# Kernel optimization log

Measured on AMD Instinct MI355X. Metric: run time of the kernel, lower is better.

## Reference

```python
import jax, jax.numpy as jnp
import numpy as np


def setup_inputs() -> dict:
    key = jax.random.key(0)
    ks = jax.random.split(key, 10)
    B, T, D = 256, 256, 256
    CH, L, K = 128, 3, 10          # chunk_size, levels, conv_size
    H = CH * L                     # hidden_dim = 384
    G = 4 * H + 2 * L              # gate projection width = 1542
    HS = H // 6

    def xavier(k, shape):
        fan_in, fan_out = shape[0], shape[-1]
        lim = np.sqrt(6.0 / (fan_in + fan_out)).astype(np.float32)
        return jax.random.uniform(k, shape, jnp.float32, -lim, lim)

    x = jax.random.normal(ks[0], (B, T, D), jnp.float32)
    lengths = jax.random.randint(ks[1], (B,), 1, T + 1).astype(jnp.int64)
    Wk = xavier(ks[2], (D + 1, G)); bk = jnp.zeros((G,), jnp.float32)
    Wr = xavier(ks[3], (H + 1, G)); br = jnp.zeros((G,), jnp.float32)
    Ws = xavier(ks[4], (H, HS));    bs = jnp.zeros((HS,), jnp.float32)
    Wrs = xavier(ks[5], (HS, H));   brs = jnp.zeros((H,), jnp.float32)
    Wc = xavier(ks[6], (H, H, K)) / np.sqrt(K)  # Conv1d weight (out, in, k)
    bc = jnp.zeros((H,), jnp.float32)
    return {"x": x, "lengths": lengths, "Wk": Wk, "bk": bk, "Wr": Wr,
            "br": br, "Ws": Ws, "bs": bs, "Wrs": Wrs, "brs": brs,
            "Wc": Wc, "bc": bc}


def _cumax_l2r(z):
    return jnp.cumsum(jax.nn.softmax(z, axis=-1), axis=-1)


def _cumax_r2l(z):
    zf = jnp.flip(z, -1)
    return jnp.flip(jnp.cumsum(jax.nn.softmax(zf, axis=-1), axis=-1), -1)


def reference(x, lengths, Wk, bk, Wr, br, Ws, bs, Wrs, brs, Wc, bc):
    B, T, D = x.shape
    H = Wr.shape[0] - 1
    G = Wk.shape[1]
    L = (G - 4 * H) // 2
    CH = H // L
    K = Wc.shape[2]
    ones = jnp.ones((B, 1), x.dtype)

    def step(carry, xt):
        c, h, tmp_h, tmp_dis = carry
        # two linear projections (interval == 1 always)
        xo = (jnp.concatenate([xt, ones], -1) @ Wk + bk
              + jnp.concatenate([h, ones], -1) @ Wr + br)
        fm = _cumax_l2r(xo[:, :L])[:, :, None]          # (B,L,1)
        im = _cumax_r2l(xo[:, L:2 * L])[:, :, None]     # (B,L,1)
        rest = xo[:, 2 * L:].reshape(B, 4 * L, CH)
        f = jax.nn.sigmoid(rest[:, :L])
        i = jax.nn.sigmoid(rest[:, L:2 * L])
        o = jax.nn.sigmoid(rest[:, 2 * L:3 * L])
        c_in = jnp.tanh(rest[:, 3 * L:])
        c_last = c.reshape(B, L, CH)
        ov = fm * im
        c_new = (ov * (f * c_last + i * c_in)
                 + (fm - ov) * c_last + (im - ov) * c_in)
        h_new = (o * jnp.tanh(c_new)).reshape(B, H)
        c_new = c_new.reshape(B, H)
        cur_dis = 1.0 - jnp.mean(fm[..., 0], axis=-1)   # (B,)
        # sliding buffers (K, B, H) and (K, B)
        tmp_h = jnp.concatenate([tmp_h[1:], h_new[None]], 0)
        tmp_dis = jnp.concatenate([tmp_dis[1:], cur_dis[None]], 0)
        # local window attention weights
        ld = jax.nn.softmax(jnp.cumsum(tmp_dis.T, axis=1), axis=1)  # (B,K)
        local_h = tmp_h.transpose(1, 2, 0) * ld[:, None, :]         # (B,H,K)
        theme = jax.nn.sigmoid(
            jax.nn.relu(jnp.mean(local_h, -1) @ Ws + bs) @ Wrs + brs)
        conv = jnp.einsum('bhk,ohk->bo', local_h, Wc) + bc          # valid conv -> len 1
        local_out = theme * conv
        return (c_new, h_new, tmp_h, tmp_dis), (h_new, local_out)

    c0 = jnp.zeros((B, H), x.dtype)
    h0 = jnp.zeros((B, H), x.dtype)
    th0 = jnp.zeros((K, B, H), x.dtype)
    td0 = jnp.zeros((K, B), x.dtype)
    _, (origin_h, loc_h) = jax.lax.scan(step, (c0, h0, th0, td0),
                                        x.transpose(1, 0, 2))
    output = (loc_h + origin_h).transpose(1, 0, 2)   # (B,T,H)
    idx = jnp.clip(lengths, 1, T).astype(jnp.int32) - 1
    last_output = output[jnp.arange(B), idx]
    return (last_output, output)
```

## Files before the change

kernel.cpp:

```cpp
#include <hip/hip_runtime.h>
#include <hip/hip_bf16.h>
#include <cstddef>

#define B_  256
#define T_  256
#define D_  256
#define H_  384
#define G_  1542
#define L_  3
#define CH_ 128
#define K_  10
#define HS_ 64

#define NGRP 16
#define NMEM 16
#define GW   16
#define CPM  24
#define NFR  7
#define PCOLS 112
#define XOLP 114
#define NKC  20
#define STG_BYTES 12288
#define XOL_OFF   STG_BYTES
#define LDS_BYTES (STG_BYTES + XOLP * GW * 4)

#define POST_LDS 107520

#define SENT 0xFFFFFFFFFFFFFFFFull

using bf16x8 = __attribute__((ext_vector_type(8))) short;
using f32x4  = __attribute__((ext_vector_type(4))) float;
typedef unsigned long long ull_t;

__device__ __forceinline__ float bf2f(unsigned short s) {
    return __uint_as_float(((unsigned)s) << 16);
}
__device__ __forceinline__ unsigned short f2bf(float f) {
    unsigned u = __float_as_uint(f);
    return (unsigned short)((u + 0x7fffu + ((u >> 16) & 1u)) >> 16);
}
__device__ __forceinline__ float sig_fast(float x) { return 1.f / (1.f + __expf(-x)); }
__device__ __forceinline__ float tanh_fast(float x) {
    float ax = fabsf(x);
    float t = __expf(-2.f * ax);
    float r = (1.f - t) / (1.f + t);
    return copysignf(r, x);
}
__device__ __forceinline__ ull_t ldA(const ull_t* p) {
    return __hip_atomic_load(p, __ATOMIC_RELAXED, __HIP_MEMORY_SCOPE_AGENT);
}
__device__ __forceinline__ bool rdy(ull_t v) {
    ull_t x = ~v;
    return (((x - 0x0001000100010001ull) & ~x & 0x8000800080008000ull) == 0ull);
}

__device__ __forceinline__ int gcol_of(int member, int p) {
    if (p < 6) return p;
    if (p < 102) { int q = p - 6; return 6 + (q / CPM) * H_ + member * CPM + (q % CPM); }
    return -1;
}

__global__ __launch_bounds__(256)
void k_xa(const float* __restrict__ x, unsigned short* __restrict__ xA) {
    __shared__ float xl[64][261];
    const int t = blockIdx.x, bq = blockIdx.y;
    const int b0 = bq * 64, tid = threadIdx.x;
    for (int idx = tid; idx < 4096; idx += 256) {
        int row = idx >> 6, c4 = idx & 63;
        float4 v = *(const float4*)(x + ((size_t)(b0 + row) * T_ + t) * D_ + c4 * 4);
        xl[row][c4 * 4 + 0] = v.x; xl[row][c4 * 4 + 1] = v.y;
        xl[row][c4 * 4 + 2] = v.z; xl[row][c4 * 4 + 3] = v.w;
    }
    __syncthreads();
    for (int idx = tid; idx < 2048; idx += 256) {
        int lane = idx & 63, gl = (idx >> 6) & 3, kc = idx >> 8;
        int brow = gl * 16 + (lane & 15);
        int d = kc * 32 + (lane >> 4) * 8;
        unsigned o[4];
        #pragma unroll
        for (int q = 0; q < 4; ++q)
            o[q] = (unsigned)f2bf(xl[brow][d + 2 * q])
                 | ((unsigned)f2bf(xl[brow][d + 2 * q + 1]) << 16);
        int4 pk = make_int4((int)o[0], (int)o[1], (int)o[2], (int)o[3]);
        ((int4*)xA)[(((size_t)t * 8 + kc) * 16 + (bq * 4 + gl)) * 64 + lane] = pk;
    }
}

__global__ __launch_bounds__(256)
void k_prep(const float* __restrict__ Wk, const float* __restrict__ bk,
            const float* __restrict__ Wr, const float* __restrict__ br,
            const float* __restrict__ Ws, const float* __restrict__ Wrs,
            const float* __restrict__ Wc,
            unsigned short* __restrict__ hbf, unsigned short* __restrict__ Wf,
            unsigned short* __restrict__ Wg, unsigned short* __restrict__ WsT,
            unsigned short* __restrict__ WrsT, float* __restrict__ biasP)
{
    const int bid = blockIdx.x, tid = threadIdx.x;
    if (bid < 2048) {
        ull_t* hb = (ull_t*)hbf;
        int base = bid * 256 + tid;
        #pragma unroll
        for (int j = 0; j < 12; ++j)
            __hip_atomic_store(hb + base + j * 524288, SENT,
                               __ATOMIC_RELAXED, __HIP_MEMORY_SCOPE_AGENT);
    } else if (bid < 2608) {
        int idx = (bid - 2048) * 256 + tid;
        int lane = idx & 63;
        int ni   = (idx >> 6) % NFR;
        int kc   = (idx / (64 * NFR)) % NKC;
        int member = idx / (64 * NFR * NKC);
        int p = ni * 16 + (lane & 15);
        int g = gcol_of(member, p);
        unsigned short out[8];
        #pragma unroll
        for (int j = 0; j < 8; ++j) {
            int k = kc * 32 + (lane >> 4) * 8 + j;
            float v = 0.f;
            if (g >= 0) v = (k < 256) ? Wk[(size_t)k * G_ + g] : Wr[(size_t)(k - 256) * G_ + g];
            out[j] = f2bf(v);
        }
        int4 pk;
        pk.x = (unsigned)out[0] | ((unsigned)out[1] << 16);
        pk.y = (unsigned)out[2] | ((unsigned)out[3] << 16);
        pk.z = (unsigned)out[4] | ((unsigned)out[5] << 16);
        pk.w = (unsigned)out[6] | ((unsigned)out[7] << 16);
        ((int4*)Wf)[idx] = pk;
    } else if (bid < 8368) {
        int idx = (bid - 2608) * 256 + tid;
        int o = idx / (K_ * H_);
        int rem = idx % (K_ * H_);
        int k = rem / H_, h = rem % H_;
        Wg[idx] = f2bf(Wc[((size_t)o * H_ + h) * K_ + k]);
    } else if (bid < 8464) {
        int idx = (bid - 8368) * 256 + tid;
        int jj = idx / H_, k = idx % H_;
        WsT[idx] = f2bf(Ws[(size_t)k * HS_ + jj]);
    } else if (bid < 8560) {
        int idx = (bid - 8464) * 256 + tid;
        int o = idx / HS_, jj = idx % HS_;
        WrsT[idx] = f2bf(Wrs[(size_t)jj * H_ + o]);
    } else {
        int idx = (bid - 8560) * 256 + tid;
        if (idx < NMEM * PCOLS) {
            int member = idx / PCOLS, p = idx % PCOLS;
            int g = gcol_of(member, p);
            biasP[idx] = (g >= 0)
                ? bk[g] + br[g] + Wk[(size_t)256 * G_ + g] + Wr[(size_t)384 * G_ + g] : 0.f;
        }
    }
}

__global__ __launch_bounds__(512, 1)
void k_serial(const unsigned short* __restrict__ xA, const unsigned short* __restrict__ Wf,
              const float* __restrict__ biasP,
              unsigned short* __restrict__ hbf, float* __restrict__ dis)
{
    extern __shared__ char lds_raw[];
    int4* stage4 = (int4*)lds_raw;
    const bf16x8* stage = (const bf16x8*)lds_raw;
    float* xol = (float*)(lds_raw + XOL_OFF);

    const int tid = threadIdx.x;
    const int lane = tid & 63, wave = tid >> 6;
    const int group = blockIdx.x & 15, member = blockIdx.x >> 4;
    const int b0 = group * GW;
    const int ni = wave;
    const bool domm = (wave < NFR);

    bf16x8 wreg[NKC];
    if (domm) {
        const bf16x8* wsrc = (const bf16x8*)(Wf + (size_t)member * (NKC * NFR * 64 * 8));
        #pragma unroll
        for (int kc = 0; kc < NKC; ++kc)
            wreg[kc] = wsrc[(kc * NFR + ni) * 64 + lane];
    }
    const float bias_a = domm ? biasP[member * PCOLS + ni * 16 + (lane & 15)] : 0.f;

    const bool hasS = (tid < 384);
    const int skcl = tid >> 6, sln = tid & 63;
    const int stA = skcl * 64 + sln;
    const int stB = (skcl + 6) * 64 + sln;
    const unsigned short* src0 =
        hbf + (size_t)(b0 + (sln & 15)) * H_ + skcl * 32 + (sln >> 4) * 8;

    float c_r0 = 0.f;

    for (int t = 0; t < T_; ++t) {
        bf16x8 xf[8];
        if (domm) {
            #pragma unroll
            for (int kc = 0; kc < 8; ++kc)
                xf[kc] = *((const bf16x8*)(xA
                    + (((size_t)t * 8 + kc) * 16 + group) * 512 + lane * 8));
        }

        f32x4 accA = f32x4{bias_a, bias_a, bias_a, bias_a};
        f32x4 accB = f32x4{0.f, 0.f, 0.f, 0.f};

        if (t > 0) {
            const size_t toff = (size_t)(t - 1) * B_ * H_;
            const ull_t* pA = (const ull_t*)(src0 + toff);
            const ull_t* pB = (const ull_t*)(src0 + toff + 192);
            ull_t v0 = SENT, v1 = SENT, v2 = SENT, v3 = SENT;
            if (hasS) { v0 = ldA(pA); v1 = ldA(pA + 1); v2 = ldA(pB); v3 = ldA(pB + 1); }

            if (domm) {
                #pragma unroll
                for (int kc = 0; kc < 8; ++kc) {
                    if (kc & 1)
                        accB = __builtin_amdgcn_mfma_f32_16x16x32_bf16(xf[kc], wreg[kc], accB, 0, 0, 0);
                    else
                        accA = __builtin_amdgcn_mfma_f32_16x16x32_bf16(xf[kc], wreg[kc], accA, 0, 0, 0);
                }
            }

            if (hasS) {
                while (!(rdy(v0) && rdy(v1) && rdy(v2) && rdy(v3))) {
                    v0 = ldA(pA); v1 = ldA(pA + 1); v2 = ldA(pB); v3 = ldA(pB + 1);
                }
                stage4[stA] = make_int4((int)(v0 & 0xffffffffu), (int)(v0 >> 32),
                                        (int)(v1 & 0xffffffffu), (int)(v1 >> 32));
                stage4[stB] = make_int4((int)(v2 & 0xffffffffu), (int)(v2 >> 32),
                                        (int)(v3 & 0xffffffffu), (int)(v3 >> 32));
            }
            __syncthreads();
            if (domm) {
                #pragma unroll
                for (int kcl = 0; kcl < 12; ++kcl) {
                    bf16x8 a0 = stage[kcl * 64 + lane];
                    if (kcl & 1)
                        accB = __builtin_amdgcn_mfma_f32_16x16x32_bf16(a0, wreg[8 + kcl], accB, 0, 0, 0);
                    else
                        accA = __builtin_amdgcn_mfma_f32_16x16x32_bf16(a0, wreg[8 + kcl], accA, 0, 0, 0);
                }
            }
        } else {
            if (domm) {
                #pragma unroll
                for (int kc = 0; kc < 8; ++kc) {
                    if (kc & 1)
                        accB = __builtin_amdgcn_mfma_f32_16x16x32_bf16(xf[kc], wreg[kc], accB, 0, 0, 0);
                    else
                        accA = __builtin_amdgcn_mfma_f32_16x16x32_bf16(xf[kc], wreg[kc], accA, 0, 0, 0);
                }
            }
        }

        if (domm) {
            #pragma unroll
            for (int r = 0; r < 4; ++r)
                xol[((lane >> 4) * 4 + r) * XOLP + ni * 16 + (lane & 15)] = accA[r] + accB[r];
        }
        __syncthreads();

        if (tid < 384) {
            int b = tid & 15, ch = tid >> 4;
            const float* row = xol + b * XOLP;
            float z0 = row[0], z1 = row[1], z2 = row[2];
            float z3 = row[3], z4 = row[4], z5 = row[5];
            float m1 = fmaxf(fmaxf(z0, z1), z2);
            float e0 = __expf(z0 - m1), e1 = __expf(z1 - m1), e2 = __expf(z2 - m1);
            float inv1 = 1.f / (e0 + e1 + e2);
            float fm0 = e0 * inv1, fm1 = (e0 + e1) * inv1;
            float m2 = fmaxf(fmaxf(z3, z4), z5);
            float f3 = __expf(z3 - m2), f4 = __expf(z4 - m2), f5 = __expf(z5 - m2);
            float inv2 = 1.f / (f3 + f4 + f5);
            float im1 = (f4 + f5) * inv2, im2 = f5 * inv2;

            int hh = member * CPM + ch;
            int l = hh >> 7;
            float fm = (l == 0) ? fm0 : (l == 1) ? fm1 : 1.f;
            float im = (l == 0) ? 1.f : (l == 1) ? im1 : im2;

            float fg = sig_fast(row[6 + ch]);
            float ig = sig_fast(row[6 + CPM + ch]);
            float og = sig_fast(row[6 + 2 * CPM + ch]);
            float ci = tanh_fast(row[6 + 3 * CPM + ch]);

            float ov = fm * im;
            float cn = ov * (fg * c_r0 + ig * ci) + (fm - ov) * c_r0 + (im - ov) * ci;
            float hn = og * tanh_fast(cn);
            c_r0 = cn;

            unsigned hpk = (unsigned)f2bf(hn);
            unsigned partner = (unsigned)__shfl((int)hpk, (lane + 16) & 63);
            if (!(ch & 1)) {
                unsigned word = hpk | (partner << 16);
                __hip_atomic_store(
                    (unsigned*)(hbf + ((size_t)t * B_ + b0 + b) * H_ + hh),
                    word, __ATOMIC_RELAXED, __HIP_MEMORY_SCOPE_AGENT);
            }
            if (member == 0 && ch == 0)
                dis[t * B_ + b0 + b] = 1.f - (fm0 + fm1 + 1.f) * (1.f / 3.f);
        }
    }
}

__global__ __launch_bounds__(512, 1)
void k_post(const unsigned short* __restrict__ hbf, const float* __restrict__ dis,
            const unsigned short* __restrict__ Wg,
            const unsigned short* __restrict__ WsT, const unsigned short* __restrict__ WrsT,
            const float* __restrict__ bs, const float* __restrict__ brs,
            const float* __restrict__ bc, float* __restrict__ out_part)
{
    extern __shared__ char plds[];
    float* ldl = (float*)plds;
    unsigned short* AlB = (unsigned short*)(plds + 5120);
    unsigned short* BlB = (unsigned short*)(plds + 46080);
    unsigned short* hbarL = (unsigned short*)(plds + 5120);
    unsigned short* uL = (unsigned short*)(plds + 56320);

    const int bid = blockIdx.x + 4 * blockIdx.y;
    const int xcd = bid & 7, slot = bid >> 3;
    const int tpair = xcd * 16 + (slot >> 2);
    const int btile = slot & 3;
    const int b0 = btile * 64;
    const int t0 = tpair * 2;
    const int tid = threadIdx.x;
    const int wave = tid >> 6, lane = tid & 63;
    const int mh = wave >> 2, nq = wave & 3;

    if (tid < 128) {
        int ti = tid >> 6, bi = tid & 63;
        int t = t0 + ti, b = b0 + bi;
        float s = 0.f, sk[K_];
        #pragma unroll
        for (int k = 0; k < K_; ++k) {
            int tau = t - (K_ - 1) + k;
            float d = (tau >= 0) ? dis[tau * B_ + b] : 0.f;
            s += d; sk[k] = s;
        }
        float m = sk[0];
        #pragma unroll
        for (int k = 1; k < K_; ++k) m = fmaxf(m, sk[k]);
        float sum = 0.f;
        #pragma unroll
        for (int k = 0; k < K_; ++k) { sk[k] = __expf(sk[k] - m); sum += sk[k]; }
        float inv = 1.f / sum;
        #pragma unroll
        for (int k = 0; k < K_; ++k) ldl[ti * 640 + bi * 10 + k] = sk[k] * inv;
    }

    const int a_ti = tid >> 8, a_rem = tid & 255;
    const int a_bb = a_rem >> 2, a_half = a_rem & 3;

    auto loadA = [&](int ch, int4& av, bool& valid) {
        int k = ch / 12, hb = (ch % 12) * 32;
        int tau = t0 + a_ti - (K_ - 1) + k;
        valid = (tau >= 0);
        if (valid)
            av = *(const int4*)(hbf + ((size_t)tau * B_ + b0 + a_bb) * H_ + hb + a_half * 8);
    };
    auto loadB = [&](int ch, int4 bv[3]) {
        #pragma unroll
        for (int q = 0; q < 3; ++q) {
            int idx = q * 512 + tid;
            int row = idx >> 2, half = idx & 3;
            bv[q] = *(const int4*)(Wg + (size_t)row * 3840 + ch * 32 + half * 8);
        }
    };
    auto writeA = [&](int buf, int ch, int4 av, bool valid) {
        int k = ch / 12;
        int4 pk = make_int4(0, 0, 0, 0);
        if (valid) {
            float l = ldl[a_ti * 640 + a_bb * 10 + k];
            unsigned vv[4] = {(unsigned)av.x, (unsigned)av.y, (unsigned)av.z, (unsigned)av.w};
            unsigned o[4];
            #pragma unroll
            for (int q = 0; q < 4; ++q) {
                float flo = __uint_as_float(vv[q] << 16) * l;
                float fhi = __uint_as_float(vv[q] & 0xffff0000u) * l;
                o[q] = (unsigned)f2bf(flo) | ((unsigned)f2bf(fhi) << 16);
            }
            pk = make_int4((int)o[0], (int)o[1], (int)o[2], (int)o[3]);
        }
        *(int4*)&AlB[buf * 5120 + a_ti * 2560 + a_bb * 40 + a_half * 8] = pk;
    };
    auto writeB = [&](int buf, const int4 bv[3]) {
        #pragma unroll
        for (int q = 0; q < 3; ++q) {
            int idx = q * 512 + tid;
            int row = idx >> 2, half = idx & 3;
            *(int4*)&BlB[buf * 15360 + row * 40 + half * 8] = bv[q];
        }
    };

    int4 av; bool avalid; int4 bv[3];
    loadA(0, av, avalid); loadB(0, bv);
    __syncthreads();
    writeA(0, 0, av, avalid); writeB(0, bv);

    f32x4 acc[2][2][6] = {};
    for (int ch = 0; ch < 120; ++ch) {
        int cur = ch & 1;
        bool more = (ch + 1 < 120);
        if (more) { loadA(ch + 1, av, avalid); loadB(ch + 1, bv); }
        __syncthreads();
        if (more) { writeA(cur ^ 1, ch + 1, av, avalid); writeB(cur ^ 1, bv); }

        bf16x8 af[2][2];
        #pragma unroll
        for (int ti = 0; ti < 2; ++ti)
            #pragma unroll
            for (int mi = 0; mi < 2; ++mi)
                af[ti][mi] = *(const bf16x8*)&AlB[cur * 5120 + ti * 2560
                    + (mh * 32 + mi * 16 + (lane & 15)) * 40 + (lane >> 4) * 8];
        #pragma unroll
        for (int ni = 0; ni < 6; ++ni) {
            bf16x8 bfv = *(const bf16x8*)&BlB[cur * 15360
                + (nq * 96 + ni * 16 + (lane & 15)) * 40 + (lane >> 4) * 8];
            #pragma unroll
            for (int ti = 0; ti < 2; ++ti)
                #pragma unroll
                for (int mi = 0; mi < 2; ++mi)
                    acc[ti][mi][ni] = __builtin_amdgcn_mfma_f32_16x16x32_bf16(
                        af[ti][mi], bfv, acc[ti][mi][ni], 0, 0, 0);
        }
    }
    __syncthreads();

    #pragma unroll
    for (int ti = 0; ti < 2; ++ti) {
        const int t = t0 + ti;
        for (int idx = tid; idx < 3072; idx += 512) {
            int bb = idx / 48, h8 = idx % 48;
            float s[8] = {};
            #pragma unroll
            for (int k = 0; k < K_; ++k) {
                int tau = t - (K_ - 1) + k;
                if (tau >= 0) {
                    int4 v = *(const int4*)(hbf + ((size_t)tau * B_ + b0 + bb) * H_ + h8 * 8);
                    float l = ldl[ti * 640 + bb * 10 + k];
                    unsigned vv[4] = {(unsigned)v.x, (unsigned)v.y, (unsigned)v.z, (unsigned)v.w};
                    #pragma unroll
                    for (int q = 0; q < 4; ++q) {
                        s[2 * q]     = fmaf(__uint_as_float(vv[q] << 16), l, s[2 * q]);
                        s[2 * q + 1] = fmaf(__uint_as_float(vv[q] & 0xffff0000u), l, s[2 * q + 1]);
                    }
                }
            }
            unsigned o[4];
            #pragma unroll
            for (int q = 0; q < 4; ++q)
                o[q] = (unsigned)f2bf(s[2 * q] * 0.1f) | ((unsigned)f2bf(s[2 * q + 1] * 0.1f) << 16);
            *(int4*)&hbarL[bb * 400 + h8 * 8] = make_int4((int)o[0], (int)o[1], (int)o[2], (int)o[3]);
        }
        __syncthreads();

        if (wave < 4) {
            f32x4 uacc[4] = {};
            for (int kc = 0; kc < 12; ++kc) {
                bf16x8 a = *(const bf16x8*)&hbarL[(wave * 16 + (lane & 15)) * 400
                                                  + kc * 32 + (lane >> 4) * 8];
                #pragma unroll
                for (int ni = 0; ni < 4; ++ni) {
                    bf16x8 wb = *(const bf16x8*)(WsT + (size_t)(ni * 16 + (lane & 15)) * H_
                                                 + kc * 32 + (lane >> 4) * 8);
                    uacc[ni] = __builtin_amdgcn_mfma_f32_16x16x32_bf16(a, wb, uacc[ni], 0, 0, 0);
                }
            }
            #pragma unroll
            for (int ni = 0; ni < 4; ++ni) {
                float bsv = bs[ni * 16 + (lane & 15)];
                #pragma unroll
                for (int r = 0; r < 4; ++r)
                    uL[(wave * 16 + (lane >> 4) * 4 + r) * 72 + ni * 16 + (lane & 15)] =
                        f2bf(fmaxf(uacc[ni][r] + bsv, 0.f));
            }
        }
        __syncthreads();

        #pragma unroll
        for (int half = 0; half < 2; ++half) {
            f32x4 tacc[2][3] = {};
            #pragma unroll
            for (int kc = 0; kc < 2; ++kc) {
                bf16x8 ua[2];
                #pragma unroll
                for (int mi = 0; mi < 2; ++mi)
                    ua[mi] = *(const bf16x8*)&uL[(mh * 32 + mi * 16 + (lane & 15)) * 72
                                                 + kc * 32 + (lane >> 4) * 8];
                #pragma unroll
                for (int n3 = 0; n3 < 3; ++n3) {
                    int ni = half * 3 + n3;
                    bf16x8 wb = *(const bf16x8*)(WrsT
                        + (size_t)(nq * 96 + ni * 16 + (lane & 15)) * HS_
                        + kc * 32 + (lane >> 4) * 8);
                    #pragma unroll
                    for (int mi = 0; mi < 2; ++mi)
                        tacc[mi][n3] = __builtin_amdgcn_mfma_f32_16x16x32_bf16(
                            ua[mi], wb, tacc[mi][n3], 0, 0, 0);
                }
            }
            #pragma unroll
            for (int mi = 0; mi < 2; ++mi) {
                #pragma unroll
                for (int n3 = 0; n3 < 3; ++n3) {
                    int ni = half * 3 + n3;
                    int o = nq * 96 + ni * 16 + (lane & 15);
                    float brsv = brs[o], bcv = bc[o];
                    int brow0 = b0 + mh * 32 + mi * 16 + ((lane >> 4) << 2);
                    #pragma unroll
                    for (int r = 0; r < 4; ++r) {
                        float th = sig_fast(tacc[mi][n3][r] + brsv);
                        float cv = acc[ti][mi][ni][r] + bcv;
                        float hv = bf2f(hbf[((size_t)t * B_ + brow0 + r) * H_ + o]);
                        __builtin_nontemporal_store(hv + th * cv,
                            out_part + ((size_t)(brow0 + r) * T_ + t) * H_ + o);
                    }
                }
            }
        }
        __syncthreads();
    }
}

__global__ void k_last(const int* __restrict__ len_i, const float* __restrict__ out_part,
                       float* __restrict__ last)
{
    int b = blockIdx.x, tid = threadIdx.x;
    bool is64 = (len_i[1] == 0);
    long long v = is64 ? ((const long long*)len_i)[b] : (long long)len_i[b];
    int idx = (int)v;
    idx = max(1, min(T_, idx)) - 1;
    last[(size_t)b * H_ + tid] = out_part[((size_t)b * T_ + idx) * H_ + tid];
}

extern "C" void kernel_launch(void* const* d_in, const int* in_sizes, int n_in,
                              void* d_out, int out_size, void* d_ws, size_t ws_size,
                              hipStream_t stream) {
    const float* x   = (const float*)d_in[0];
    const int*   len = (const int*)d_in[1];
    const float* Wk  = (const float*)d_in[2];
    const float* bk  = (const float*)d_in[3];
    const float* Wr  = (const float*)d_in[4];
    const float* br  = (const float*)d_in[5];
    const float* Ws  = (const float*)d_in[6];
    const float* bs  = (const float*)d_in[7];
    const float* Wrs = (const float*)d_in[8];
    const float* brs = (const float*)d_in[9];
    const float* Wc  = (const float*)d_in[10];
    const float* bc  = (const float*)d_in[11];

    float* out      = (float*)d_out;
    float* last     = out;
    float* out_part = out + (size_t)B_ * H_;

    char* p = (char*)d_ws;
    float*          dis    = (float*)p;          p += (size_t)T_ * B_ * 4;
    unsigned short* xA     = (unsigned short*)p; p += (size_t)T_ * B_ * D_ * 2;
    unsigned short* WfragG = (unsigned short*)p; p += (size_t)NMEM * NKC * NFR * 64 * 8 * 2;
    float*          biasP  = (float*)p;          p += (size_t)NMEM * PCOLS * 4;
    unsigned short* hbf    = (unsigned short*)p; p += (size_t)T_ * B_ * H_ * 2;
    unsigned short* Wg     = (unsigned short*)p; p += (size_t)H_ * K_ * H_ * 2;
    unsigned short* WsT    = (unsigned short*)p; p += (size_t)HS_ * H_ * 2;
    unsigned short* WrsT   = (unsigned short*)p; p += (size_t)H_ * HS_ * 2;

    k_xa  <<<dim3(T_, 4), 256, 0, stream>>>(x, xA);
    k_prep<<<8567, 256, 0, stream>>>(Wk, bk, Wr, br, Ws, Wrs, Wc,
                                     hbf, WfragG, Wg, WsT, WrsT, biasP);

    hipFuncSetAttribute((const void*)k_serial,
                        hipFuncAttributeMaxDynamicSharedMemorySize, LDS_BYTES);
    hipFuncSetAttribute((const void*)k_post,
                        hipFuncAttributeMaxDynamicSharedMemorySize, POST_LDS);

    k_serial<<<NGRP * NMEM, 512, LDS_BYTES, stream>>>(xA, WfragG, biasP, hbf, dis);
    k_post <<<dim3(4, 128), 512, POST_LDS, stream>>>(hbf, dis, Wg, WsT, WrsT, bs, brs, bc, out_part);
    k_last <<<B_, H_, 0, stream>>>(len, out_part, last);
}
```

Before: 1.245 ms.

## Fuse serial recurrence and post-processing into one kernel with progress flags

Merges the serial recurrence kernel and the local-window post kernel into a single 512-block launch. The first 256 blocks run the recurrence and publish a per-group progress counter after each timestep. The remaining blocks wait on those counters and run the conv/theme post-processing for finished timesteps, so that work overlaps with the serial chain instead of running after it. The post stage's LDS budget is shrunk to fit (smaller B staging buffer) so both roles fit in one launch. This risks spin-wait contention and relies on all blocks being co-resident.

```diff
diff --git a/kernel.cpp b/kernel.cpp
--- a/kernel.cpp
+++ b/kernel.cpp
@@ -22,9 +22,7 @@
 #define NKC  20
 #define STG_BYTES 12288
 #define XOL_OFF   STG_BYTES
-#define LDS_BYTES (STG_BYTES + XOLP * GW * 4)
-
-#define POST_LDS 107520
+#define MAIN_LDS 65536
 
 #define SENT 0xFFFFFFFFFFFFFFFFull
 
@@ -93,7 +91,8 @@
             const float* __restrict__ Wc,
             unsigned short* __restrict__ hbf, unsigned short* __restrict__ Wf,
             unsigned short* __restrict__ Wg, unsigned short* __restrict__ WsT,
-            unsigned short* __restrict__ WrsT, float* __restrict__ biasP)
+            unsigned short* __restrict__ WrsT, float* __restrict__ biasP,
+            unsigned* __restrict__ progress)
 {
     const int bid = blockIdx.x, tid = threadIdx.x;
     if (bid < 2048) {
@@ -139,7 +138,7 @@
         int idx = (bid - 8464) * 256 + tid;
         int o = idx / HS_, jj = idx % HS_;
         WrsT[idx] = f2bf(Wrs[(size_t)jj * H_ + o]);
-    } else {
+    } else if (bid < 8567) {
         int idx = (bid - 8560) * 256 + tid;
         if (idx < NMEM * PCOLS) {
             int member = idx / PCOLS, p = idx % PCOLS;
@@ -147,371 +146,388 @@
             biasP[idx] = (g >= 0)
                 ? bk[g] + br[g] + Wk[(size_t)256 * G_ + g] + Wr[(size_t)384 * G_ + g] : 0.f;
         }
+    } else {
+        if (tid < NGRP * NMEM)
+            __hip_atomic_store(progress + tid, 0u,
+                               __ATOMIC_RELAXED, __HIP_MEMORY_SCOPE_AGENT);
     }
 }
 
 __global__ __launch_bounds__(512, 1)
-void k_serial(const unsigned short* __restrict__ xA, const unsigned short* __restrict__ Wf,
-              const float* __restrict__ biasP,
-              unsigned short* __restrict__ hbf, float* __restrict__ dis)
-{
-    extern __shared__ char lds_raw[];
-    int4* stage4 = (int4*)lds_raw;
-    const bf16x8* stage = (const bf16x8*)lds_raw;
-    float* xol = (float*)(lds_raw + XOL_OFF);
-
-    const int tid = threadIdx.x;
-    const int lane = tid & 63, wave = tid >> 6;
-    const int group = blockIdx.x & 15, member = blockIdx.x >> 4;
-    const int b0 = group * GW;
-    const int ni = wave;
-    const bool domm = (wave < NFR);
-
-    bf16x8 wreg[NKC];
-    if (domm) {
-        const bf16x8* wsrc = (const bf16x8*)(Wf + (size_t)member * (NKC * NFR * 64 * 8));
-        #pragma unroll
-        for (int kc = 0; kc < NKC; ++kc)
-            wreg[kc] = wsrc[(kc * NFR + ni) * 64 + lane];
-    }
-    const float bias_a = domm ? biasP[member * PCOLS + ni * 16 + (lane & 15)] : 0.f;
-
-    const bool hasS = (tid < 384);
-    const int skcl = tid >> 6, sln = tid & 63;
-    const int stA = skcl * 64 + sln;
-    const int stB = (skcl + 6) * 64 + sln;
-    const unsigned short* src0 =
-        hbf + (size_t)(b0 + (sln & 15)) * H_ + skcl * 32 + (sln >> 4) * 8;
-
-    float c_r0 = 0.f;
-
-    for (int t = 0; t < T_; ++t) {
-        bf16x8 xf[8];
-        if (domm) {
-            #pragma unroll
-            for (int kc = 0; kc < 8; ++kc)
-                xf[kc] = *((const bf16x8*)(xA
-                    + (((size_t)t * 8 + kc) * 16 + group) * 512 + lane * 8));
-        }
-
-        f32x4 accA = f32x4{bias_a, bias_a, bias_a, bias_a};
-        f32x4 accB = f32x4{0.f, 0.f, 0.f, 0.f};
-
-        if (t > 0) {
-            const size_t toff = (size_t)(t - 1) * B_ * H_;
-            const ull_t* pA = (const ull_t*)(src0 + toff);
-            const ull_t* pB = (const ull_t*)(src0 + toff + 192);
-            ull_t v0 = SENT, v1 = SENT, v2 = SENT, v3 = SENT;
-            if (hasS) { v0 = ldA(pA); v1 = ldA(pA + 1); v2 = ldA(pB); v3 = ldA(pB + 1); }
-
-            if (domm) {
-                #pragma unroll
-                for (int kc = 0; kc < 8; ++kc) {
-                    if (kc & 1)
-                        accB = __builtin_amdgcn_mfma_f32_16x16x32_bf16(xf[kc], wreg[kc], accB, 0, 0, 0);
-                    else
-                        accA = __builtin_amdgcn_mfma_f32_16x16x32_bf16(xf[kc], wreg[kc], accA, 0, 0, 0);
-                }
-            }
-
-            if (hasS) {
-                while (!(rdy(v0) && rdy(v1) && rdy(v2) && rdy(v3))) {
-                    v0 = ldA(pA); v1 = ldA(pA + 1); v2 = ldA(pB); v3 = ldA(pB + 1);
-                }
-                stage4[stA] = make_int4((int)(v0 & 0xffffffffu), (int)(v0 >> 32),
-                                        (int)(v1 & 0xffffffffu), (int)(v1 >> 32));
-                stage4[stB] = make_int4((int)(v2 & 0xffffffffu), (int)(v2 >> 32),
-                                        (int)(v3 & 0xffffffffu), (int)(v3 >> 32));
-            }
-            __syncthreads();
-            if (domm) {
-                #pragma unroll
-                for (int kcl = 0; kcl < 12; ++kcl) {
-                    bf16x8 a0 = stage[kcl * 64 + lane];
-                    if (kcl & 1)
-                        accB = __builtin_amdgcn_mfma_f32_16x16x32_bf16(a0, wreg[8 + kcl], accB, 0, 0, 0);
-                    else
-                        accA = __builtin_amdgcn_mfma_f32_16x16x32_bf16(a0, wreg[8 + kcl], accA, 0, 0, 0);
-                }
-            }
-        } else {
-            if (domm) {
-                #pragma unroll
-                for (int kc = 0; kc < 8; ++kc) {
-                    if (kc & 1)
-                        accB = __builtin_amdgcn_mfma_f32_16x16x32_bf16(xf[kc], wreg[kc], accB, 0, 0, 0);
-                    else
-                        accA = __builtin_amdgcn_mfma_f32_16x16x32_bf16(xf[kc], wreg[kc], accA, 0, 0, 0);
-                }
-            }
-        }
-
-        if (domm) {
-            #pragma unroll
-            for (int r = 0; r < 4; ++r)
-                xol[((lane >> 4) * 4 + r) * XOLP + ni * 16 + (lane & 15)] = accA[r] + accB[r];
-        }
-        __syncthreads();
-
-        if (tid < 384) {
-            int b = tid & 15, ch = tid >> 4;
-            const float* row = xol + b * XOLP;
-            float z0 = row[0], z1 = row[1], z2 = row[2];
-            float z3 = row[3], z4 = row[4], z5 = row[5];
-            float m1 = fmaxf(fmaxf(z0, z1), z2);
-            float e0 = __expf(z0 - m1), e1 = __expf(z1 - m1), e2 = __expf(z2 - m1);
-            float inv1 = 1.f / (e0 + e1 + e2);
-            float fm0 = e0 * inv1, fm1 = (e0 + e1) * inv1;
-            float m2 = fmaxf(fmaxf(z3, z4), z5);
-            float f3 = __expf(z3 - m2), f4 = __expf(z4 - m2), f5 = __expf(z5 - m2);
-            float inv2 = 1.f / (f3 + f4 + f5);
-            float im1 = (f4 + f5) * inv2, im2 = f5 * inv2;
-
-            int hh = member * CPM + ch;
-            int l = hh >> 7;
-            float fm = (l == 0) ? fm0 : (l == 1) ? fm1 : 1.f;
-            float im = (l == 0) ? 1.f : (l == 1) ? im1 : im2;
-
-            float fg = sig_fast(row[6 + ch]);
-            float ig = sig_fast(row[6 + CPM + ch]);
-            float og = sig_fast(row[6 + 2 * CPM + ch]);
-            float ci = tanh_fast(row[6 + 3 * CPM + ch]);
-
-            float ov = fm * im;
-            float cn = ov * (fg * c_r0 + ig * ci) + (fm - ov) * c_r0 + (im - ov) * ci;
-            float hn = og * tanh_fast(cn);
-            c_r0 = cn;
-
-            unsigned hpk = (unsigned)f2bf(hn);
-            unsigned partner = (unsigned)__shfl((int)hpk, (lane + 16) & 63);
-            if (!(ch & 1)) {
-                unsigned word = hpk | (partner << 16);
-                __hip_atomic_store(
-                    (unsigned*)(hbf + ((size_t)t * B_ + b0 + b) * H_ + hh),
-                    word, __ATOMIC_RELAXED, __HIP_MEMORY_SCOPE_AGENT);
-            }
-            if (member == 0 && ch == 0)
-                dis[t * B_ + b0 + b] = 1.f - (fm0 + fm1 + 1.f) * (1.f / 3.f);
-        }
-    }
-}
-
-__global__ __launch_bounds__(512, 1)
-void k_post(const unsigned short* __restrict__ hbf, const float* __restrict__ dis,
+void k_main(const unsigned short* __restrict__ xA, const unsigned short* __restrict__ Wf,
+            const float* __restrict__ biasP, unsigned short* __restrict__ hbf,
+            float* __restrict__ dis, unsigned* __restrict__ progress,
             const unsigned short* __restrict__ Wg,
             const unsigned short* __restrict__ WsT, const unsigned short* __restrict__ WrsT,
             const float* __restrict__ bs, const float* __restrict__ brs,
             const float* __restrict__ bc, float* __restrict__ out_part)
 {
-    extern __shared__ char plds[];
-    float* ldl = (float*)plds;
-    unsigned short* AlB = (unsigned short*)(plds + 5120);
-    unsigned short* BlB = (unsigned short*)(plds + 46080);
-    unsigned short* hbarL = (unsigned short*)(plds + 5120);
-    unsigned short* uL = (unsigned short*)(plds + 56320);
-
-    const int bid = blockIdx.x + 4 * blockIdx.y;
-    const int xcd = bid & 7, slot = bid >> 3;
-    const int tpair = xcd * 16 + (slot >> 2);
-    const int btile = slot & 3;
-    const int b0 = btile * 64;
-    const int t0 = tpair * 2;
+    extern __shared__ char lds_raw[];
     const int tid = threadIdx.x;
-    const int wave = tid >> 6, lane = tid & 63;
+    const int lane = tid & 63, wave = tid >> 6;
+
+    if (blockIdx.x < 256) {
+        int4* stage4 = (int4*)lds_raw;
+        const bf16x8* stage = (const bf16x8*)lds_raw;
+        float* xol = (float*)(lds_raw + XOL_OFF);
+
+        const int group = blockIdx.x & 15, member = blockIdx.x >> 4;
+        const int b0 = group * GW;
+        const int ni = wave;
+        const bool domm = (wave < NFR);
+
+        bf16x8 wreg[NKC];
+        if (domm) {
+            const bf16x8* wsrc = (const bf16x8*)(Wf + (size_t)member * (NKC * NFR * 64 * 8));
+            #pragma unroll
+            for (int kc = 0; kc < NKC; ++kc)
+                wreg[kc] = wsrc[(kc * NFR + ni) * 64 + lane];
+        }
+        const float bias_a = domm ? biasP[member * PCOLS + ni * 16 + (lane & 15)] : 0.f;
+
+        const bool hasS = (tid < 384);
+        const int skcl = tid >> 6, sln = tid & 63;
+        const int stA = skcl * 64 + sln;
+        const int stB = (skcl + 6) * 64 + sln;
+        const unsigned short* src0 =
+            hbf + (size_t)(b0 + (sln & 15)) * H_ + skcl * 32 + (sln >> 4) * 8;
+
+        float c_r0 = 0.f;
+
+        for (int t = 0; t < T_; ++t) {
+            bf16x8 xf[8];
+            if (domm) {
+                #pragma unroll
+                for (int kc = 0; kc < 8; ++kc)
+                    xf[kc] = *((const bf16x8*)(xA
+                        + (((size_t)t * 8 + kc) * 16 + group) * 512 + lane * 8));
+            }
+
+            f32x4 accA = f32x4{bias_a, bias_a, bias_a, bias_a};
+            f32x4 accB = f32x4{0.f, 0.f, 0.f, 0.f};
+
+            if (t > 0) {
+                const size_t toff = (size_t)(t - 1) * B_ * H_;
+                const ull_t* pA = (const ull_t*)(src0 + toff);
+                const ull_t* pB = (const ull_t*)(src0 + toff + 192);
+                ull_t v0 = SENT, v1 = SENT, v2 = SENT, v3 = SENT;
+                if (hasS) { v0 = ldA(pA); v1 = ldA(pA + 1); v2 = ldA(pB); v3 = ldA(pB + 1); }
+
+                if (domm) {
+                    #pragma unroll
+                    for (int kc = 0; kc < 8; ++kc) {
+                        if (kc & 1)
+                            accB = __builtin_amdgcn_mfma_f32_16x16x32_bf16(xf[kc], wreg[kc], accB, 0, 0, 0);
+                        else
+                            accA = __builtin_amdgcn_mfma_f32_16x16x32_bf16(xf[kc], wreg[kc], accA, 0, 0, 0);
+                    }
+                }
+
+                if (hasS) {
+                    while (!(rdy(v0) && rdy(v1) && rdy(v2) && rdy(v3))) {
+                        v0 = ldA(pA); v1 = ldA(pA + 1); v2 = ldA(pB); v3 = ldA(pB + 1);
+                    }
+                    stage4[stA] = make_int4((int)(v0 & 0xffffffffu), (int)(v0 >> 32),
+                                            (int)(v1 & 0xffffffffu), (int)(v1 >> 32));
+                    stage4[stB] = make_int4((int)(v2 & 0xffffffffu), (int)(v2 >> 32),
+                                            (int)(v3 & 0xffffffffu), (int)(v3 >> 32));
+                }
+                __syncthreads();
+                if (domm) {
+                    #pragma unroll
+                    for (int kcl = 0; kcl < 12; ++kcl) {
+                        bf16x8 a0 = stage[kcl * 64 + lane];
+                        if (kcl & 1)
+                            accB = __builtin_amdgcn_mfma_f32_16x16x32_bf16(a0, wreg[8 + kcl], accB, 0, 0, 0);
+                        else
+                            accA = __builtin_amdgcn_mfma_f32_16x16x32_bf16(a0, wreg[8 + kcl], accA, 0, 0, 0);
+                    }
+                }
+            } else {
+                if (domm) {
+                    #pragma unroll
+                    for (int kc = 0; kc < 8; ++kc) {
+                        if (kc & 1)
+                            accB = __builtin_amdgcn_mfma_f32_16x16x32_bf16(xf[kc], wreg[kc], accB, 0, 0, 0);
+                        else
+                            accA = __builtin_amdgcn_mfma_f32_16x16x32_bf16(xf[kc], wreg[kc], accA, 0, 0, 0);
+                    }
+                }
+            }
+
+            if (domm) {
+                #pragma unroll
+                for (int r = 0; r < 4; ++r)
+                    xol[((lane >> 4) * 4 + r) * XOLP + ni * 16 + (lane & 15)] = accA[r] + accB[r];
+            }
+            __syncthreads();
+
+            if (tid < 384) {
+                int b = tid & 15, ch = tid >> 4;
+                const float* row = xol + b * XOLP;
+                float z0 = row[0], z1 = row[1], z2 = row[2];
+                float z3 = row[3], z4 = row[4], z5 = row[5];
+                float m1 = fmaxf(fmaxf(z0, z1), z2);
+                float e0 = __expf(z0 - m1), e1 = __expf(z1 - m1), e2 = __expf(z2 - m1);
+                float inv1 = 1.f / (e0 + e1 + e2);
+                float fm0 = e0 * inv1, fm1 = (e0 + e1) * inv1;
+                float m2 = fmaxf(fmaxf(z3, z4), z5);
+                float f3 = __expf(z3 - m2), f4 = __expf(z4 - m2), f5 = __expf(z5 - m2);
+                float inv2 = 1.f / (f3 + f4 + f5);
+                float im1 = (f4 + f5) * inv2, im2 = f5 * inv2;
+
+                int hh = member * CPM + ch;
+                int l = hh >> 7;
+                float fm = (l == 0) ? fm0 : (l == 1) ? fm1 : 1.f;
+                float im = (l == 0) ? 1.f : (l == 1) ? im1 : im2;
+
+                float fg = sig_fast(row[6 + ch]);
+                float ig = sig_fast(row[6 + CPM + ch]);
+                float og = sig_fast(row[6 + 2 * CPM + ch]);
+                float ci = tanh_fast(row[6 + 3 * CPM + ch]);
+
+                float ov = fm * im;
+                float cn = ov * (fg * c_r0 + ig * ci) + (fm - ov) * c_r0 + (im - ov) * ci;
+                float hn = og * tanh_fast(cn);
+                c_r0 = cn;
+
+                unsigned hpk = (unsigned)f2bf(hn);
+                unsigned partner = (unsigned)__shfl((int)hpk, (lane + 16) & 63);
+                if (!(ch & 1)) {
+                    unsigned word = hpk | (partner << 16);
+                    __hip_atomic_store(
+                        (unsigned*)(hbf + ((size_t)t * B_ + b0 + b) * H_ + hh),
+                        word, __ATOMIC_RELAXED, __HIP_MEMORY_SCOPE_AGENT);
+                }
+                if (member == 0 && ch == 0)
+                    __hip_atomic_store(dis + t * B_ + b0 + b,
+                        1.f - (fm0 + fm1 + 1.f) * (1.f / 3.f),
+                        __ATOMIC_RELAXED, __HIP_MEMORY_SCOPE_AGENT);
+            }
+            __syncthreads();
+            if (tid == 0)
+                __hip_atomic_store(progress + group * NMEM + member, (unsigned)(t + 1),
+                                   __ATOMIC_RELAXED, __HIP_MEMORY_SCOPE_AGENT);
+        }
+        return;
+    }
+
+    float* ldl = (float*)lds_raw;
+    unsigned short* Al = (unsigned short*)(lds_raw + 5120);
+    unsigned short* Bl = (unsigned short*)(lds_raw + 15360);
+    unsigned short* hbarL = (unsigned short*)(lds_raw + 5120);
+    unsigned short* uL = (unsigned short*)(lds_raw + 56320);
+
+    const int p0 = (int)blockIdx.x - 256;
     const int mh = wave >> 2, nq = wave & 3;
 
-    if (tid < 128) {
-        int ti = tid >> 6, bi = tid & 63;
-        int t = t0 + ti, b = b0 + bi;
-        float s = 0.f, sk[K_];
-        #pragma unroll
-        for (int k = 0; k < K_; ++k) {
-            int tau = t - (K_ - 1) + k;
-            float d = (tau >= 0) ? dis[tau * B_ + b] : 0.f;
-            s += d; sk[k] = s;
-        }
-        float m = sk[0];
-        #pragma unroll
-        for (int k = 1; k < K_; ++k) m = fmaxf(m, sk[k]);
-        float sum = 0.f;
-        #pragma unroll
-        for (int k = 0; k < K_; ++k) { sk[k] = __expf(sk[k] - m); sum += sk[k]; }
-        float inv = 1.f / sum;
-        #pragma unroll
-        for (int k = 0; k < K_; ++k) ldl[ti * 640 + bi * 10 + k] = sk[k] * inv;
-    }
-
-    const int a_ti = tid >> 8, a_rem = tid & 255;
-    const int a_bb = a_rem >> 2, a_half = a_rem & 3;
-
-    auto loadA = [&](int ch, int4& av, bool& valid) {
-        int k = ch / 12, hb = (ch % 12) * 32;
-        int tau = t0 + a_ti - (K_ - 1) + k;
-        valid = (tau >= 0);
-        if (valid)
-            av = *(const int4*)(hbf + ((size_t)tau * B_ + b0 + a_bb) * H_ + hb + a_half * 8);
-    };
-    auto loadB = [&](int ch, int4 bv[3]) {
-        #pragma unroll
-        for (int q = 0; q < 3; ++q) {
-            int idx = q * 512 + tid;
-            int row = idx >> 2, half = idx & 3;
-            bv[q] = *(const int4*)(Wg + (size_t)row * 3840 + ch * 32 + half * 8);
-        }
-    };
-    auto writeA = [&](int buf, int ch, int4 av, bool valid) {
-        int k = ch / 12;
-        int4 pk = make_int4(0, 0, 0, 0);
-        if (valid) {
-            float l = ldl[a_ti * 640 + a_bb * 10 + k];
-            unsigned vv[4] = {(unsigned)av.x, (unsigned)av.y, (unsigned)av.z, (unsigned)av.w};
-            unsigned o[4];
-            #pragma unroll
-            for (int q = 0; q < 4; ++q) {
-                float flo = __uint_as_float(vv[q] << 16) * l;
-                float fhi = __uint_as_float(vv[q] & 0xffff0000u) * l;
-                o[q] = (unsigned)f2bf(flo) | ((unsigned)f2bf(fhi) << 16);
-            }
-            pk = make_int4((int)o[0], (int)o[1], (int)o[2], (int)o[3]);
-        }
-        *(int4*)&AlB[buf * 5120 + a_ti * 2560 + a_bb * 40 + a_half * 8] = pk;
-    };
-    auto writeB = [&](int buf, const int4 bv[3]) {
-        #pragma unroll
-        for (int q = 0; q < 3; ++q) {
-            int idx = q * 512 + tid;
-            int row = idx >> 2, half = idx & 3;
-            *(int4*)&BlB[buf * 15360 + row * 40 + half * 8] = bv[q];
-        }
-    };
-
-    int4 av; bool avalid; int4 bv[3];
-    loadA(0, av, avalid); loadB(0, bv);
-    __syncthreads();
-    writeA(0, 0, av, avalid); writeB(0, bv);
-
-    f32x4 acc[2][2][6] = {};
-    for (int ch = 0; ch < 120; ++ch) {
-        int cur = ch & 1;
-        bool more = (ch + 1 < 120);
-        if (more) { loadA(ch + 1, av, avalid); loadB(ch + 1, bv); }
+    for (int tile = p0; tile < 512; tile += 256) {
+        const int tpair = tile >> 2, btile = tile & 3;
+        const int t0 = tpair * 2;
+        const int b0 = btile * 64;
+
+        if (tid < 64) {
+            int g = btile * 4 + (tid >> 4), m = tid & 15;
+            const unsigned need = (unsigned)(t0 + 2);
+            while (__hip_atomic_load(progress + g * NMEM + m,
+                                     __ATOMIC_RELAXED, __HIP_MEMORY_SCOPE_AGENT) < need)
+                __builtin_amdgcn_s_sleep(8);
+        }
         __syncthreads();
-        if (more) { writeA(cur ^ 1, ch + 1, av, avalid); writeB(cur ^ 1, bv); }
-
-        bf16x8 af[2][2];
-        #pragma unroll
-        for (int ti = 0; ti < 2; ++ti)
-            #pragma unroll
-            for (int mi = 0; mi < 2; ++mi)
-                af[ti][mi] = *(const bf16x8*)&AlB[cur * 5120 + ti * 2560
-                    + (mh * 32 + mi * 16 + (lane & 15)) * 40 + (lane >> 4) * 8];
-        #pragma unroll
-        for (int ni = 0; ni < 6; ++ni) {
-            bf16x8 bfv = *(const bf16x8*)&BlB[cur * 15360
-                + (nq * 96 + ni * 16 + (lane & 15)) * 40 + (lane >> 4) * 8];
-            #pragma unroll
-            for (int ti = 0; ti < 2; ++ti)
-                #pragma unroll
-                for (int mi = 0; mi < 2; ++mi)
-                    acc[ti][mi][ni] = __builtin_amdgcn_mfma_f32_16x16x32_bf16(
-                        af[ti][mi], bfv, acc[ti][mi][ni], 0, 0, 0);
-        }
-    }
-    __syncthreads();
-
-    #pragma unroll
-    for (int ti = 0; ti < 2; ++ti) {
-        const int t = t0 + ti;
-        for (int idx = tid; idx < 3072; idx += 512) {
-            int bb = idx / 48, h8 = idx % 48;
-            float s[8] = {};
+
+        if (tid < 128) {
+            int ti = tid >> 6, bi = tid & 63;
+            int t = t0 + ti, b = b0 + bi;
+            float s = 0.f, sk[K_];
             #pragma unroll
             for (int k = 0; k < K_; ++k) {
                 int tau = t - (K_ - 1) + k;
-                if (tau >= 0) {
-                    int4 v = *(const int4*)(hbf + ((size_t)tau * B_ + b0 + bb) * H_ + h8 * 8);
-                    float l = ldl[ti * 640 + bb * 10 + k];
-                    unsigned vv[4] = {(unsigned)v.x, (unsigned)v.y, (unsigned)v.z, (unsigned)v.w};
-                    #pragma unroll
-                    for (int q = 0; q < 4; ++q) {
-                        s[2 * q]     = fmaf(__uint_as_float(vv[q] << 16), l, s[2 * q]);
-                        s[2 * q + 1] = fmaf(__uint_as_float(vv[q] & 0xffff0000u), l, s[2 * q + 1]);
-                    }
-                }
-            }
-            unsigned o[4];
-            #pragma unroll
-            for (int q = 0; q < 4; ++q)
-                o[q] = (unsigned)f2bf(s[2 * q] * 0.1f) | ((unsigned)f2bf(s[2 * q + 1] * 0.1f) << 16);
-            *(int4*)&hbarL[bb * 400 + h8 * 8] = make_int4((int)o[0], (int)o[1], (int)o[2], (int)o[3]);
-        }
+                float d = (tau >= 0) ? dis[tau * B_ + b] : 0.f;
+                s += d; sk[k] = s;
+            }
+            float m = sk[0];
+            #pragma unroll
+            for (int k = 1; k < K_; ++k) m = fmaxf(m, sk[k]);
+            float sum = 0.f;
+            #pragma unroll
+            for (int k = 0; k < K_; ++k) { sk[k] = __expf(sk[k] - m); sum += sk[k]; }
+            float inv = 1.f / sum;
+            #pragma unroll
+            for (int k = 0; k < K_; ++k) ldl[ti * 640 + bi * 10 + k] = sk[k] * inv;
+        }
+
+        const int a_ti = tid >> 8, a_rem = tid & 255;
+        const int a_bb = a_rem >> 2, a_half = a_rem & 3;
+
+        auto loadA = [&](int ch, int4& av, bool& valid) {
+            int k = ch / 12, hb = (ch % 12) * 32;
+            int tau = t0 + a_ti - (K_ - 1) + k;
+            valid = (tau >= 0);
+            if (valid)
+                av = *(const int4*)(hbf + ((size_t)tau * B_ + b0 + a_bb) * H_ + hb + a_half * 8);
+        };
+        auto loadB = [&](int ch, int4 bv[3]) {
+            #pragma unroll
+            for (int q = 0; q < 3; ++q) {
+                int idx = q * 512 + tid;
+                int row = idx >> 2, half = idx & 3;
+                bv[q] = *(const int4*)(Wg + (size_t)row * 3840 + ch * 32 + half * 8);
+            }
+        };
+        auto writeA = [&](int ch, int4 av, bool valid) {
+            int k = ch / 12;
+            int4 pk = make_int4(0, 0, 0, 0);
+            if (valid) {
+                float l = ldl[a_ti * 640 + a_bb * 10 + k];
+                unsigned vv[4] = {(unsigned)av.x, (unsigned)av.y, (unsigned)av.z, (unsigned)av.w};
+                unsigned o[4];
+                #pragma unroll
+                for (int q = 0; q < 4; ++q) {
+                    float flo = __uint_as_float(vv[q] << 16) * l;
+                    float fhi = __uint_as_float(vv[q] & 0xffff0000u) * l;
+                    o[q] = (unsigned)f2bf(flo) | ((unsigned)f2bf(fhi) << 16);
+                }
+                pk = make_int4((int)o[0], (int)o[1], (int)o[2], (int)o[3]);
+            }
+            *(int4*)&Al[a_ti * 2560 + a_bb * 40 + a_half * 8] = pk;
+        };
+        auto writeB = [&](const int4 bv[3]) {
+            #pragma unroll
+            for (int q = 0; q < 3; ++q) {
+                int idx = q * 512 + tid;
+                int row = idx >> 2, half = idx & 3;
+                *(int4*)&Bl[row * 40 + half * 8] = bv[q];
+            }
+        };
+
+        int4 av; bool avalid; int4 bv[3];
+        loadA(0, av, avalid); loadB(0, bv);
         __syncthreads();
-
-        if (wave < 4) {
-            f32x4 uacc[4] = {};
-            for (int kc = 0; kc < 12; ++kc) {
-                bf16x8 a = *(const bf16x8*)&hbarL[(wave * 16 + (lane & 15)) * 400
-                                                  + kc * 32 + (lane >> 4) * 8];
+        writeA(0, av, avalid); writeB(bv);
+
+        f32x4 acc[2][2][6] = {};
+        for (int ch = 0; ch < 120; ++ch) {
+            bool more = (ch + 1 < 120);
+            if (more) { loadA(ch + 1, av, avalid); loadB(ch + 1, bv); }
+            __syncthreads();
+
+            bf16x8 af[2][2];
+            #pragma unroll
+            for (int ti = 0; ti < 2; ++ti)
+                #pragma unroll
+                for (int mi = 0; mi < 2; ++mi)
+                    af[ti][mi] = *(const bf16x8*)&Al[ti * 2560
+                        + (mh * 32 + mi * 16 + (lane & 15)) * 40 + (lane >> 4) * 8];
+            #pragma unroll
+            for (int ni = 0; ni < 6; ++ni) {
+                bf16x8 bfv = *(const bf16x8*)&Bl[(nq * 96 + ni * 16 + (lane & 15)) * 40
+                                                 + (lane >> 4) * 8];
+                #pragma unroll
+                for (int ti = 0; ti < 2; ++ti)
+                    #pragma unroll
+                    for (int mi = 0; mi < 2; ++mi)
+                        acc[ti][mi][ni] = __builtin_amdgcn_mfma_f32_16x16x32_bf16(
+                            af[ti][mi], bfv, acc[ti][mi][ni], 0, 0, 0);
+            }
+            __syncthreads();
+            if (more) { writeA(ch + 1, av, avalid); writeB(bv); }
+        }
+        __syncthreads();
+
+        #pragma unroll
+        for (int ti = 0; ti < 2; ++ti) {
+            const int t = t0 + ti;
+            for (int idx = tid; idx < 3072; idx += 512) {
+                int bb = idx / 48, h8 = idx % 48;
+                float s[8] = {};
+                #pragma unroll
+                for (int k = 0; k < K_; ++k) {
+                    int tau = t - (K_ - 1) + k;
+                    if (tau >= 0) {
+                        int4 v = *(const int4*)(hbf + ((size_t)tau * B_ + b0 + bb) * H_ + h8 * 8);
+                        float l = ldl[ti * 640 + bb * 10 + k];
+                        unsigned vv[4] = {(unsigned)v.x, (unsigned)v.y, (unsigned)v.z, (unsigned)v.w};
+                        #pragma unroll
+                        for (int q = 0; q < 4; ++q) {
+                            s[2 * q]     = fmaf(__uint_as_float(vv[q] << 16), l, s[2 * q]);
+                            s[2 * q + 1] = fmaf(__uint_as_float(vv[q] & 0xffff0000u), l, s[2 * q + 1]);
+                        }
+                    }
+                }
+                unsigned o[4];
+                #pragma unroll
+                for (int q = 0; q < 4; ++q)
+                    o[q] = (unsigned)f2bf(s[2 * q] * 0.1f) | ((unsigned)f2bf(s[2 * q + 1] * 0.1f) << 16);
+                *(int4*)&hbarL[bb * 400 + h8 * 8] = make_int4((int)o[0], (int)o[1], (int)o[2], (int)o[3]);
+            }
+            __syncthreads();
+
+            if (wave < 4) {
+                f32x4 uacc[4] = {};
+                for (int kc = 0; kc < 12; ++kc) {
+                    bf16x8 a = *(const bf16x8*)&hbarL[(wave * 16 + (lane & 15)) * 400
+                                                      + kc * 32 + (lane >> 4) * 8];
+                    #pragma unroll
+                    for (int ni = 0; ni < 4; ++ni) {
+                        bf16x8 wb = *(const bf16x8*)(WsT + (size_t)(ni * 16 + (lane & 15)) * H_
+                                                     + kc * 32 + (lane >> 4) * 8);
+                        uacc[ni] = __builtin_amdgcn_mfma_f32_16x16x32_bf16(a, wb, uacc[ni], 0, 0, 0);
+                    }
+                }
                 #pragma unroll
                 for (int ni = 0; ni < 4; ++ni) {
-                    bf16x8 wb = *(const bf16x8*)(WsT + (size_t)(ni * 16 + (lane & 15)) * H_
-                                                 + kc * 32 + (lane >> 4) * 8);
-                    uacc[ni] = __builtin_amdgcn_mfma_f32_16x16x32_bf16(a, wb, uacc[ni], 0, 0, 0);
-                }
-            }
-            #pragma unroll
-            for (int ni = 0; ni < 4; ++ni) {
-                float bsv = bs[ni * 16 + (lane & 15)];
-                #pragma unroll
-                for (int r = 0; r < 4; ++r)
-                    uL[(wave * 16 + (lane >> 4) * 4 + r) * 72 + ni * 16 + (lane & 15)] =
-                        f2bf(fmaxf(uacc[ni][r] + bsv, 0.f));
-            }
-        }
-        __syncthreads();
-
-        #pragma unroll
-        for (int half = 0; half < 2; ++half) {
-            f32x4 tacc[2][3] = {};
-            #pragma unroll
-            for (int kc = 0; kc < 2; ++kc) {
-                bf16x8 ua[2];
-                #pragma unroll
-                for (int mi = 0; mi < 2; ++mi)
-                    ua[mi] = *(const bf16x8*)&uL[(mh * 32 + mi * 16 + (lane & 15)) * 72
-                                                 + kc * 32 + (lane >> 4) * 8];
-                #pragma unroll
-                for (int n3 = 0; n3 < 3; ++n3) {
-                    int ni = half * 3 + n3;
-                    bf16x8 wb = *(const bf16x8*)(WrsT
-                        + (size_t)(nq * 96 + ni * 16 + (lane & 15)) * HS_
-                        + kc * 32 + (lane >> 4) * 8);
+                    float bsv = bs[ni * 16 + (lane & 15)];
+                    #pragma unroll
+                    for (int r = 0; r < 4; ++r)
+                        uL[(wave * 16 + (lane >> 4) * 4 + r) * 72 + ni * 16 + (lane & 15)] =
+                            f2bf(fmaxf(uacc[ni][r] + bsv, 0.f));
+                }
+            }
+            __syncthreads();
+
+            #pragma unroll
+            for (int half = 0; half < 2; ++half) {
+                f32x4 tacc[2][3] = {};
+                #pragma unroll
+                for (int kc = 0; kc < 2; ++kc) {
+                    bf16x8 ua[2];
                     #pragma unroll
                     for (int mi = 0; mi < 2; ++mi)
-                        tacc[mi][n3] = __builtin_amdgcn_mfma_f32_16x16x32_bf16(
-                            ua[mi], wb, tacc[mi][n3], 0, 0, 0);
-                }
-            }
-            #pragma unroll
-            for (int mi = 0; mi < 2; ++mi) {
-                #pragma unroll
-                for (int n3 = 0; n3 < 3; ++n3) {
-                    int ni = half * 3 + n3;
-                    int o = nq * 96 + ni * 16 + (lane & 15);
-                    float brsv = brs[o], bcv = bc[o];
-                    int brow0 = b0 + mh * 32 + mi * 16 + ((lane >> 4) << 2);
-                    #pragma unroll
-                    for (int r = 0; r < 4; ++r) {
-                        float th = sig_fast(tacc[mi][n3][r] + brsv);
-                        float cv = acc[ti][mi][ni][r] + bcv;
-                        float hv = bf2f(hbf[((size_t)t * B_ + brow0 + r) * H_ + o]);
-                        __builtin_nontemporal_store(hv + th * cv,
-                            out_part + ((size_t)(brow0 + r) * T_ + t) * H_ + o);
-                    }
-                }
-            }
-        }
-        __syncthreads();
+                        ua[mi] = *(const bf16x8*)&uL[(mh * 32 + mi * 16 + (lane & 15)) * 72
+                                                     + kc * 32 + (lane >> 4) * 8];
+                    #pragma unroll
+                    for (int n3 = 0; n3 < 3; ++n3) {
+                        int ni = half * 3 + n3;
+                        bf16x8 wb = *(const bf16x8*)(WrsT
+                            + (size_t)(nq * 96 + ni * 16 + (lane & 15)) * HS_
+                            + kc * 32 + (lane >> 4) * 8);
+                        #pragma unroll
+                        for (int mi = 0; mi < 2; ++mi)
+                            tacc[mi][n3] = __builtin_amdgcn_mfma_f32_16x16x32_bf16(
+                                ua[mi], wb, tacc[mi][n3], 0, 0, 0);
+                    }
+                }
+                #pragma unroll
+                for (int mi = 0; mi < 2; ++mi) {
+                    #pragma unroll
+                    for (int n3 = 0; n3 < 3; ++n3) {
+                        int ni = half * 3 + n3;
+                        int o = nq * 96 + ni * 16 + (lane & 15);
+                        float brsv = brs[o], bcv = bc[o];
+                        int brow0 = b0 + mh * 32 + mi * 16 + ((lane >> 4) << 2);
+                        #pragma unroll
+                        for (int r = 0; r < 4; ++r) {
+                            float th = sig_fast(tacc[mi][n3][r] + brsv);
+                            float cv = acc[ti][mi][ni][r] + bcv;
+                            float hv = bf2f(hbf[((size_t)t * B_ + brow0 + r) * H_ + o]);
+                            __builtin_nontemporal_store(hv + th * cv,
+                                out_part + ((size_t)(brow0 + r) * T_ + t) * H_ + o);
+                        }
+                    }
+                }
+            }
+            __syncthreads();
+        }
     }
 }
 
@@ -548,6 +564,7 @@
 
     char* p = (char*)d_ws;
     float*          dis    = (float*)p;          p += (size_t)T_ * B_ * 4;
+    unsigned*       progress = (unsigned*)p;     p += 1024;
     unsigned short* xA     = (unsigned short*)p; p += (size_t)T_ * B_ * D_ * 2;
     unsigned short* WfragG = (unsigned short*)p; p += (size_t)NMEM * NKC * NFR * 64 * 8 * 2;
     float*          biasP  = (float*)p;          p += (size_t)NMEM * PCOLS * 4;
@@ -557,15 +574,13 @@
     unsigned short* WrsT   = (unsigned short*)p; p += (size_t)H_ * HS_ * 2;
 
     k_xa  <<<dim3(T_, 4), 256, 0, stream>>>(x, xA);
-    k_prep<<<8567, 256, 0, stream>>>(Wk, bk, Wr, br, Ws, Wrs, Wc,
-                                     hbf, WfragG, Wg, WsT, WrsT, biasP);
-
-    hipFuncSetAttribute((const void*)k_serial,
-                        hipFuncAttributeMaxDynamicSharedMemorySize, LDS_BYTES);
-    hipFuncSetAttribute((const void*)k_post,
-                        hipFuncAttributeMaxDynamicSharedMemorySize, POST_LDS);
-
-    k_serial<<<NGRP * NMEM, 512, LDS_BYTES, stream>>>(xA, WfragG, biasP, hbf, dis);
-    k_post <<<dim3(4, 128), 512, POST_LDS, stream>>>(hbf, dis, Wg, WsT, WrsT, bs, brs, bc, out_part);
+    k_prep<<<8568, 256, 0, stream>>>(Wk, bk, Wr, br, Ws, Wrs, Wc,
+                                     hbf, WfragG, Wg, WsT, WrsT, biasP, progress);
+
+    hipFuncSetAttribute((const void*)k_main,
+                        hipFuncAttributeMaxDynamicSharedMemorySize, MAIN_LDS);
+
+    k_main<<<512, 512, MAIN_LDS, stream>>>(xA, WfragG, biasP, hbf, dis, progress,
+                                           Wg, WsT, WrsT, bs, brs, bc, out_part);
     k_last <<<B_, H_, 0, stream>>>(len, out_part, last);
 }
```

Measured after the change: 1.391 ms. 11.7% more time.
